# Kernel tuning notes

Measured on AMD Instinct MI355X. Metric: run time of the kernel, lower is better.

## Reference

```python
import jax, jax.numpy as jnp
import numpy as np

R, N1, N2, D = 4, 4096, 4096, 8


def setup_inputs() -> dict:
    key = jax.random.key(0)
    k1, k2, k3 = jax.random.split(key, 3)
    x1 = jax.random.normal(k1, (R, N1, D), dtype=jnp.float32)
    x2 = jax.random.normal(k2, (R, N2, D), dtype=jnp.float32)
    # learned parameters (init: ones), matching nn.Parameter(torch.ones(...))
    lengthscales = jnp.ones((D, 1), dtype=jnp.float32)
    output_scale = jnp.ones((1,), dtype=jnp.float32)
    return {"x1": x1, "x2": x2, "lengthscales": lengthscales, "output_scale": output_scale}


def reference(x1, x2, lengthscales, output_scale):
    # RBF.K: output_scale^2 * exp(-0.5 * sum_d ((x1 - x2) / lengthscales)^2)
    # Computed via the Gram identity ||a-b||^2 = ||a||^2 + ||b||^2 - 2 a.b
    inv_ls = 1.0 / lengthscales.reshape(-1)          # [D]
    a = x1 * inv_ls                                  # [R, N1, D]
    b = x2 * inv_ls                                  # [R, N2, D]
    aa = jnp.sum(a * a, axis=-1)                     # [R, N1]
    bb = jnp.sum(b * b, axis=-1)                     # [R, N2]
    ab = jnp.einsum('rnd,rmd->rnm', a, b)            # [R, N1, N2]
    sqdist = jnp.maximum(aa[:, :, None] + bb[:, None, :] - 2.0 * ab, 0.0)
    return (output_scale[0] ** 2) * jnp.exp(-0.5 * sqdist)
```

## Files before the change

kernel.cpp:

```cpp
#include <hip/hip_runtime.h>


constexpr int D     = 8;
constexpr int BROWS = 128;
constexpr int BJ    = 256;

#if __has_builtin(__builtin_amdgcn_exp2f)
#define FAST_EXP2(x) __builtin_amdgcn_exp2f(x)
#else
#define FAST_EXP2(x) __expf((x) * 0.69314718f)
#endif

__global__ __launch_bounds__(256, 8) void rbf_kernel(
    const float* __restrict__ x1, const float* __restrict__ x2,
    const float* __restrict__ ls, const float* __restrict__ osc,
    float* __restrict__ out, int N1, int N2)
{
    __shared__ float sb[D][BJ];
    __shared__ float sbb[BJ];
    __shared__ float sa[BROWS][D];
    __shared__ float sca[BROWS];

    const int r   = blockIdx.z;
    const int i0  = blockIdx.y * BROWS;
    const int j0  = blockIdx.x * BJ;
    const int tid = threadIdx.x;

    constexpr float L2E  = 1.44269504f;
    constexpr float NH2E = -0.72134752f;

    {
        float4 l0 = *reinterpret_cast<const float4*>(ls);
        float4 l1 = *reinterpret_cast<const float4*>(ls + 4);
        float4 inv0, inv1;
        inv0.x = 1.0f/l0.x; inv0.y = 1.0f/l0.y; inv0.z = 1.0f/l0.z; inv0.w = 1.0f/l0.w;
        inv1.x = 1.0f/l1.x; inv1.y = 1.0f/l1.y; inv1.z = 1.0f/l1.z; inv1.w = 1.0f/l1.w;

        {
            const float* src = x2 + ((size_t)r * N2 + j0 + tid) * D;
            float4 v0 = *reinterpret_cast<const float4*>(src);
            float4 v1 = *reinterpret_cast<const float4*>(src + 4);
            v0.x *= inv0.x; v0.y *= inv0.y; v0.z *= inv0.z; v0.w *= inv0.w;
            v1.x *= inv1.x; v1.y *= inv1.y; v1.z *= inv1.z; v1.w *= inv1.w;
            sb[0][tid] = v0.x; sb[1][tid] = v0.y; sb[2][tid] = v0.z; sb[3][tid] = v0.w;
            sb[4][tid] = v1.x; sb[5][tid] = v1.y; sb[6][tid] = v1.z; sb[7][tid] = v1.w;
            sbb[tid] = v0.x*v0.x + v0.y*v0.y + v0.z*v0.z + v0.w*v0.w
                     + v1.x*v1.x + v1.y*v1.y + v1.z*v1.z + v1.w*v1.w;
        }
        if (tid < BROWS) {
            const float* src = x1 + ((size_t)r * N1 + i0 + tid) * D;
            float4 v0 = *reinterpret_cast<const float4*>(src);
            float4 v1 = *reinterpret_cast<const float4*>(src + 4);
            v0.x *= inv0.x; v0.y *= inv0.y; v0.z *= inv0.z; v0.w *= inv0.w;
            v1.x *= inv1.x; v1.y *= inv1.y; v1.z *= inv1.z; v1.w *= inv1.w;
            *reinterpret_cast<float4*>(&sa[tid][0]) = v0;
            *reinterpret_cast<float4*>(&sa[tid][4]) = v1;
            sca[tid] = (v0.x*v0.x + v0.y*v0.y + v0.z*v0.z + v0.w*v0.w
                      + v1.x*v1.x + v1.y*v1.y + v1.z*v1.z + v1.w*v1.w) * NH2E;
        }
    }
    const float lg2os = __log2f(osc[0] * osc[0]);
    __syncthreads();

    const int lane = tid & 63;
    const int wv   = tid >> 6;

    float4 bd[D];
#pragma unroll
    for (int d = 0; d < D; ++d)
        bd[d] = *reinterpret_cast<const float4*>(&sb[d][lane * 4]);
    float4 cb;
    {
        const float4 bb = *reinterpret_cast<const float4*>(&sbb[lane * 4]);
        cb.x = fmaf(bb.x, NH2E, lg2os); cb.y = fmaf(bb.y, NH2E, lg2os);
        cb.z = fmaf(bb.z, NH2E, lg2os); cb.w = fmaf(bb.w, NH2E, lg2os);
    }

    float* obase = out + ((size_t)r * N1 + i0 + wv * 32) * (size_t)N2 + j0 + lane * 4;

#pragma unroll 4
    for (int ii = 0; ii < 32; ++ii) {
        const int row = wv * 32 + ii;
        const float4 a0 = *reinterpret_cast<const float4*>(&sa[row][0]);
        const float4 a1 = *reinterpret_cast<const float4*>(&sa[row][4]);
        const float  ca = sca[row];

        float p0 = 0.f, p1 = 0.f, p2 = 0.f, p3 = 0.f;
        const float a[D] = {a0.x, a0.y, a0.z, a0.w, a1.x, a1.y, a1.z, a1.w};
#pragma unroll
        for (int d = 0; d < D; ++d) {
            const float av = a[d];
            p0 = fmaf(av, bd[d].x, p0);
            p1 = fmaf(av, bd[d].y, p1);
            p2 = fmaf(av, bd[d].z, p2);
            p3 = fmaf(av, bd[d].w, p3);
        }
        float4 o;
        o.x = FAST_EXP2(fmaf(p0, L2E, ca + cb.x));
        o.y = FAST_EXP2(fmaf(p1, L2E, ca + cb.y));
        o.z = FAST_EXP2(fmaf(p2, L2E, ca + cb.z));
        o.w = FAST_EXP2(fmaf(p3, L2E, ca + cb.w));
        *reinterpret_cast<float4*>(obase + (size_t)ii * N2) = o;
    }
}

extern "C" void kernel_launch(void* const* d_in, const int* in_sizes, int n_in,
                              void* d_out, int out_size, void* d_ws, size_t ws_size,
                              hipStream_t stream) {
    (void)in_sizes; (void)n_in; (void)d_ws; (void)ws_size; (void)out_size;
    const float* x1  = (const float*)d_in[0];
    const float* x2  = (const float*)d_in[1];
    const float* ls  = (const float*)d_in[2];
    const float* osc = (const float*)d_in[3];
    float* out = (float*)d_out;

    const int R = 4, N1 = 4096, N2 = 4096;
    dim3 grid(N2 / BJ, N1 / BROWS, R);
    rbf_kernel<<<grid, dim3(256), 0, stream>>>(x1, x2, ls, osc, out, N1, N2);
}
```

Measured before the change: 55.83 us.

## Drop shared memory; give each wave a register-resident 1024-column panel

Removes the LDS staging and the block barrier. Each wavefront now loads and pre-scales its own 1024-column slice of x2 straight into registers (4 chunks of 256) and walks 32 rows of x1 read directly from global memory. The grid becomes a flat 512 blocks with launch bounds lowered to 2 blocks per CU, trading occupancy for more register reuse and fewer launches of setup work. The risk is higher register pressure and too few waves in flight to hide latency on a store-bound kernel.

```diff
diff --git a/kernel.cpp b/kernel.cpp
--- a/kernel.cpp
+++ b/kernel.cpp
@@ -2,8 +2,9 @@
 
 
 constexpr int D     = 8;
-constexpr int BROWS = 128;
-constexpr int BJ    = 256;
+constexpr int PANEL = 1024;
+constexpr int CH    = 4;
+constexpr int SEG   = 32;
 
 #if __has_builtin(__builtin_amdgcn_exp2f)
 #define FAST_EXP2(x) __builtin_amdgcn_exp2f(x)
@@ -11,96 +12,105 @@
 #define FAST_EXP2(x) __expf((x) * 0.69314718f)
 #endif
 
-__global__ __launch_bounds__(256, 8) void rbf_kernel(
+__global__ __launch_bounds__(256, 2) void rbf_kernel(
     const float* __restrict__ x1, const float* __restrict__ x2,
     const float* __restrict__ ls, const float* __restrict__ osc,
     float* __restrict__ out, int N1, int N2)
 {
-    __shared__ float sb[D][BJ];
-    __shared__ float sbb[BJ];
-    __shared__ float sa[BROWS][D];
-    __shared__ float sca[BROWS];
+    const int tid  = threadIdx.x;
+    const int lane = tid & 63;
+    const int wid  = blockIdx.x * 4 + (tid >> 6);
 
-    const int r   = blockIdx.z;
-    const int i0  = blockIdx.y * BROWS;
-    const int j0  = blockIdx.x * BJ;
-    const int tid = threadIdx.x;
+    const int panel = wid >> 9;
+    const int r     = (wid >> 7) & 3;
+    const int row0  = (wid & 127) * SEG;
 
     constexpr float L2E  = 1.44269504f;
     constexpr float NH2E = -0.72134752f;
 
-    {
-        float4 l0 = *reinterpret_cast<const float4*>(ls);
-        float4 l1 = *reinterpret_cast<const float4*>(ls + 4);
-        float4 inv0, inv1;
-        inv0.x = 1.0f/l0.x; inv0.y = 1.0f/l0.y; inv0.z = 1.0f/l0.z; inv0.w = 1.0f/l0.w;
-        inv1.x = 1.0f/l1.x; inv1.y = 1.0f/l1.y; inv1.z = 1.0f/l1.z; inv1.w = 1.0f/l1.w;
+    float4 l0 = *reinterpret_cast<const float4*>(ls);
+    float4 l1 = *reinterpret_cast<const float4*>(ls + 4);
+    float4 inv0, inv1;
+    inv0.x = 1.0f/l0.x; inv0.y = 1.0f/l0.y; inv0.z = 1.0f/l0.z; inv0.w = 1.0f/l0.w;
+    inv1.x = 1.0f/l1.x; inv1.y = 1.0f/l1.y; inv1.z = 1.0f/l1.z; inv1.w = 1.0f/l1.w;
+    const float lg2os = __log2f(osc[0] * osc[0]);
 
-        {
-            const float* src = x2 + ((size_t)r * N2 + j0 + tid) * D;
-            float4 v0 = *reinterpret_cast<const float4*>(src);
-            float4 v1 = *reinterpret_cast<const float4*>(src + 4);
+    float4 bd[CH][D];
+    float4 cb[CH];
+#pragma unroll
+    for (int c = 0; c < CH; ++c) {
+        const float* bp = x2 + ((size_t)r * N2 + panel * PANEL + c * 256 + lane * 4) * D;
+        float4 u[8];
+#pragma unroll
+        for (int p = 0; p < 4; ++p) {
+            float4 v0 = *reinterpret_cast<const float4*>(bp + p * D);
+            float4 v1 = *reinterpret_cast<const float4*>(bp + p * D + 4);
             v0.x *= inv0.x; v0.y *= inv0.y; v0.z *= inv0.z; v0.w *= inv0.w;
             v1.x *= inv1.x; v1.y *= inv1.y; v1.z *= inv1.z; v1.w *= inv1.w;
-            sb[0][tid] = v0.x; sb[1][tid] = v0.y; sb[2][tid] = v0.z; sb[3][tid] = v0.w;
-            sb[4][tid] = v1.x; sb[5][tid] = v1.y; sb[6][tid] = v1.z; sb[7][tid] = v1.w;
-            sbb[tid] = v0.x*v0.x + v0.y*v0.y + v0.z*v0.z + v0.w*v0.w
-                     + v1.x*v1.x + v1.y*v1.y + v1.z*v1.z + v1.w*v1.w;
+            u[2*p]   = v0;
+            u[2*p+1] = v1;
         }
-        if (tid < BROWS) {
-            const float* src = x1 + ((size_t)r * N1 + i0 + tid) * D;
-            float4 v0 = *reinterpret_cast<const float4*>(src);
-            float4 v1 = *reinterpret_cast<const float4*>(src + 4);
-            v0.x *= inv0.x; v0.y *= inv0.y; v0.z *= inv0.z; v0.w *= inv0.w;
-            v1.x *= inv1.x; v1.y *= inv1.y; v1.z *= inv1.z; v1.w *= inv1.w;
-            *reinterpret_cast<float4*>(&sa[tid][0]) = v0;
-            *reinterpret_cast<float4*>(&sa[tid][4]) = v1;
-            sca[tid] = (v0.x*v0.x + v0.y*v0.y + v0.z*v0.z + v0.w*v0.w
-                      + v1.x*v1.x + v1.y*v1.y + v1.z*v1.z + v1.w*v1.w) * NH2E;
+#pragma unroll
+        for (int d = 0; d < D; ++d) {
+            float4 t;
+            t.x = reinterpret_cast<const float*>(&u[0 + (d >> 2)])[d & 3];
+            t.y = reinterpret_cast<const float*>(&u[2 + (d >> 2)])[d & 3];
+            t.z = reinterpret_cast<const float*>(&u[4 + (d >> 2)])[d & 3];
+            t.w = reinterpret_cast<const float*>(&u[6 + (d >> 2)])[d & 3];
+            bd[c][d] = t;
         }
-    }
-    const float lg2os = __log2f(osc[0] * osc[0]);
-    __syncthreads();
-
-    const int lane = tid & 63;
-    const int wv   = tid >> 6;
-
-    float4 bd[D];
-#pragma unroll
-    for (int d = 0; d < D; ++d)
-        bd[d] = *reinterpret_cast<const float4*>(&sb[d][lane * 4]);
-    float4 cb;
-    {
-        const float4 bb = *reinterpret_cast<const float4*>(&sbb[lane * 4]);
-        cb.x = fmaf(bb.x, NH2E, lg2os); cb.y = fmaf(bb.y, NH2E, lg2os);
-        cb.z = fmaf(bb.z, NH2E, lg2os); cb.w = fmaf(bb.w, NH2E, lg2os);
+        float4 t;
+        t.x = u[0].x*u[0].x + u[0].y*u[0].y + u[0].z*u[0].z + u[0].w*u[0].w
+            + u[1].x*u[1].x + u[1].y*u[1].y + u[1].z*u[1].z + u[1].w*u[1].w;
+        t.y = u[2].x*u[2].x + u[2].y*u[2].y + u[2].z*u[2].z + u[2].w*u[2].w
+            + u[3].x*u[3].x + u[3].y*u[3].y + u[3].z*u[3].z + u[3].w*u[3].w;
+        t.z = u[4].x*u[4].x + u[4].y*u[4].y + u[4].z*u[4].z + u[4].w*u[4].w
+            + u[5].x*u[5].x + u[5].y*u[5].y + u[5].z*u[5].z + u[5].w*u[5].w;
+        t.w = u[6].x*u[6].x + u[6].y*u[6].y + u[6].z*u[6].z + u[6].w*u[6].w
+            + u[7].x*u[7].x + u[7].y*u[7].y + u[7].z*u[7].z + u[7].w*u[7].w;
+        cb[c].x = fmaf(t.x, NH2E, lg2os);
+        cb[c].y = fmaf(t.y, NH2E, lg2os);
+        cb[c].z = fmaf(t.z, NH2E, lg2os);
+        cb[c].w = fmaf(t.w, NH2E, lg2os);
     }
 
-    float* obase = out + ((size_t)r * N1 + i0 + wv * 32) * (size_t)N2 + j0 + lane * 4;
+    const float* xrow  = x1 + ((size_t)r * N1 + row0) * D;
+    float*       obase = out + ((size_t)r * N1 + row0) * (size_t)N2
+                             + panel * PANEL + lane * 4;
 
-#pragma unroll 4
-    for (int ii = 0; ii < 32; ++ii) {
-        const int row = wv * 32 + ii;
-        const float4 a0 = *reinterpret_cast<const float4*>(&sa[row][0]);
-        const float4 a1 = *reinterpret_cast<const float4*>(&sa[row][4]);
-        const float  ca = sca[row];
+#pragma unroll 2
+    for (int s = 0; s < SEG; ++s) {
+        float4 u0 = *reinterpret_cast<const float4*>(xrow + (size_t)s * D);
+        float4 u1 = *reinterpret_cast<const float4*>(xrow + (size_t)s * D + 4);
+        float a[D];
+        a[0] = u0.x * inv0.x; a[1] = u0.y * inv0.y;
+        a[2] = u0.z * inv0.z; a[3] = u0.w * inv0.w;
+        a[4] = u1.x * inv1.x; a[5] = u1.y * inv1.y;
+        a[6] = u1.z * inv1.z; a[7] = u1.w * inv1.w;
+        float asq = 0.f;
+#pragma unroll
+        for (int d = 0; d < D; ++d) asq = fmaf(a[d], a[d], asq);
+        const float ca = asq * NH2E;
 
-        float p0 = 0.f, p1 = 0.f, p2 = 0.f, p3 = 0.f;
-        const float a[D] = {a0.x, a0.y, a0.z, a0.w, a1.x, a1.y, a1.z, a1.w};
+        float* op = obase + (size_t)s * N2;
 #pragma unroll
-        for (int d = 0; d < D; ++d) {
-            const float av = a[d];
-            p0 = fmaf(av, bd[d].x, p0);
-            p1 = fmaf(av, bd[d].y, p1);
-            p2 = fmaf(av, bd[d].z, p2);
-            p3 = fmaf(av, bd[d].w, p3);
+        for (int c = 0; c < CH; ++c) {
+            float p0 = 0.f, p1 = 0.f, p2 = 0.f, p3 = 0.f;
+#pragma unroll
+            for (int d = 0; d < D; ++d) {
+                const float av = a[d];
+                p0 = fmaf(av, bd[c][d].x, p0);
+                p1 = fmaf(av, bd[c][d].y, p1);
+                p2 = fmaf(av, bd[c][d].z, p2);
+                p3 = fmaf(av, bd[c][d].w, p3);
+            }
+            float4 o;
+            o.x = FAST_EXP2(fmaf(p0, L2E, ca + cb[c].x));
+            o.y = FAST_EXP2(fmaf(p1, L2E, ca + cb[c].y));
+            o.z = FAST_EXP2(fmaf(p2, L2E, ca + cb[c].z));
+            o.w = FAST_EXP2(fmaf(p3, L2E, ca + cb[c].w));
+            *reinterpret_cast<float4*>(op + c * 256) = o;
         }
-        float4 o;
-        o.x = FAST_EXP2(fmaf(p0, L2E, ca + cb.x));
-        o.y = FAST_EXP2(fmaf(p1, L2E, ca + cb.y));
-        o.z = FAST_EXP2(fmaf(p2, L2E, ca + cb.z));
-        o.w = FAST_EXP2(fmaf(p3, L2E, ca + cb.w));
-        *reinterpret_cast<float4*>(obase + (size_t)ii * N2) = o;
     }
 }
 
@@ -114,7 +124,6 @@
     const float* osc = (const float*)d_in[3];
     float* out = (float*)d_out;
 
-    const int R = 4, N1 = 4096, N2 = 4096;
-    dim3 grid(N2 / BJ, N1 / BROWS, R);
-    rbf_kernel<<<grid, dim3(256), 0, stream>>>(x1, x2, ls, osc, out, N1, N2);
+    const int N1 = 4096, N2 = 4096;
+    rbf_kernel<<<dim3(512), dim3(256), 0, stream>>>(x1, x2, ls, osc, out, N1, N2);
 }
```

Result: no change. 55.18 us (-1.2%).
